# Optimization experiments

Measured on AMD Instinct MI355X. Metric: run time of the kernel, lower is better.

Reference implementation:

```python
import jax, jax.numpy as jnp
import numpy as np

HIDDEN = 2048
VOCAB = 32768
SEQ = 4608
N_CHUNKS = 9
CAP = 30.0
IGNORE = -100


def setup_inputs() -> dict:
    key = jax.random.key(0)
    k1, k2, k3 = jax.random.split(key, 3)
    weight = (jax.random.normal(k1, (VOCAB, HIDDEN), dtype=jnp.float32) * 0.02).astype(jnp.bfloat16)
    hidden = jax.random.normal(k2, (1, SEQ, HIDDEN), dtype=jnp.float32)
    input_ids = jax.random.randint(k3, (1, SEQ), 0, VOCAB)
    attention_mask = jnp.ones((1, SEQ), dtype=jnp.int32)
    return {"weight": weight, "hidden": hidden, "input_ids": input_ids,
            "attention_mask": attention_mask}


def _build_labels(input_ids, attention_mask):
    # labels[t] = input_ids[t+1], masked-out positions and the final position -> -100
    ids = input_ids[0]
    am = attention_mask[0]
    lab = jnp.where(am[1:] == 0, IGNORE, ids[1:])            # [S-1]
    lab = jnp.concatenate([lab, jnp.full((1,), IGNORE, lab.dtype)])  # [S]
    return lab


def reference(weight, hidden, input_ids, attention_mask):
    labels = _build_labels(input_ids, attention_mask)        # [S]
    x = hidden.reshape(-1, HIDDEN)                           # [S, H] fp32
    chunk = SEQ // N_CHUNKS
    xs = x.reshape(N_CHUNKS, chunk, HIDDEN)
    ls = labels.reshape(N_CHUNKS, chunk)

    wT = weight.T                                            # [H, V] bf16

    def chunk_loss(args):
        xc, lc = args                                        # [c,H], [c]
        # softcapped logits: CAP * tanh((x @ W^T) / CAP), mm in bf16
        t = jnp.tanh((xc.astype(jnp.bfloat16) @ wT) / CAP).astype(jnp.float32)  # [c,V]
        z = CAP * (t - jnp.max(t, axis=1, keepdims=True))    # stable shifted logits
        logp = z - jnp.log(jnp.sum(jnp.exp(z), axis=1, keepdims=True))
        valid = lc != IGNORE
        idx = jnp.where(valid, lc, 0)
        nll = -jnp.take_along_axis(logp, idx[:, None], axis=1)[:, 0]
        return jnp.sum(jnp.where(valid, nll, 0.0))

    losses = jax.lax.map(chunk_loss, (xs, ls))               # [N_CHUNKS]
    return jnp.sum(losses)
```

## Files before the change

### kernel.cpp

```cpp
#include <hip/hip_runtime.h>
#include <hip/hip_bf16.h>
#include <cstdint>

#define S_LEN   4608
#define HID     2048
#define VOCAB_N 32768
#define CAPV    30.0f
#define IGNORE_IDX (-100)
#define NT512   512
#define NKT     32

typedef short bf16x8 __attribute__((ext_vector_type(8)));
typedef float f32x4  __attribute__((ext_vector_type(4)));

__device__ __forceinline__ unsigned short f2bf_rtne(float f) {
    unsigned int u = __float_as_uint(f);
    unsigned int r = u + 0x7fffu + ((u >> 16) & 1u);
    return (unsigned short)(r >> 16);
}
__device__ __forceinline__ float bfr(float f) {
    unsigned int u = __float_as_uint(f);
    unsigned int r = u + 0x7fffu + ((u >> 16) & 1u);
    return __uint_as_float(r & 0xffff0000u);
}
__device__ __forceinline__ float bf_lo(unsigned int u) { return __uint_as_float(u << 16); }
__device__ __forceinline__ float bf_hi(unsigned int u) { return __uint_as_float(u & 0xffff0000u); }
__device__ __forceinline__ float bfdot2(unsigned int x, unsigned int w) {
    return bf_lo(x) * bf_lo(w) + bf_hi(x) * bf_hi(w);
}
__device__ __forceinline__ float softcap_ref(float logit) {
    float lb = bfr(logit);
    float x  = bfr(lb / CAPV);
    float e  = __expf(2.0f * x);
    float t  = bfr((e - 1.0f) / (e + 1.0f));
    return CAPV * t;
}

__global__ void cvt_kernel(const float* __restrict__ h, unsigned short* __restrict__ xb,
                           float* __restrict__ out) {
    if (blockIdx.x == 0 && threadIdx.x == 0) out[0] = 0.0f;
    int i = blockIdx.x * blockDim.x + threadIdx.x;
    float4 v = ((const float4*)h)[i];
    ushort4 o;
    o.x = f2bf_rtne(v.x); o.y = f2bf_rtne(v.y);
    o.z = f2bf_rtne(v.z); o.w = f2bf_rtne(v.w);
    ((ushort4*)xb)[i] = o;
}

__global__ __launch_bounds__(512, 2)
void gemm_lse_kernel(const unsigned short* __restrict__ X,
                     const unsigned short* __restrict__ W,
                     float* __restrict__ partL) {
    __shared__ __align__(16) unsigned short As[2][256 * 64];
    __shared__ __align__(16) unsigned short Bs[2][256 * 64];

    const int tid  = threadIdx.x;
    const int wid  = tid >> 6;
    const int lane = tid & 63;
    const int wr   = wid >> 2;
    const int wc   = wid & 3;
    const int q    = lane >> 4, l16 = lane & 15;
    const int tileM = blockIdx.x * 256;
    const int tileN = blockIdx.y * 256;

    const int srow = lane >> 3;
    const int csrc = (lane & 7) ^ srow;
    const unsigned short* Ag = X + (size_t)(tileM + wid * 8 + srow) * HID + csrc * 8;
    const unsigned short* Wg = W + (size_t)(tileN + wid * 8 + srow) * HID + csrc * 8;

    const int abase = (wr * 128 + l16) * 64;
    const int bbase = (wc * 64  + l16) * 64;
    const int koff0 = ((q    ) ^ (l16 & 7)) * 8;
    const int koff1 = ((q + 4) ^ (l16 & 7)) * 8;

    bf16x8 av[8][2], bv[4][2];
    f32x4  acc[8][4] = {};

#define STAGE_A(BUF, H, KT) do {                                                          \
    const unsigned short* _g = Ag + (size_t)(H) * 128 * HID + (size_t)(KT) * 64;          \
    __builtin_amdgcn_global_load_lds(                                                     \
        (const __attribute__((address_space(1))) void*)_g,                                \
        (__attribute__((address_space(3))) void*)&As[BUF][((H) * 128 + wid * 8) * 64],    \
        16, 0, 0);                                                                        \
    __builtin_amdgcn_global_load_lds(                                                     \
        (const __attribute__((address_space(1))) void*)(_g + (size_t)64 * HID),           \
        (__attribute__((address_space(3))) void*)&As[BUF][((H) * 128 + 64 + wid * 8) * 64],\
        16, 0, 0);                                                                        \
} while (0)

#define STAGE_B(BUF, H, KT) do {                                                          \
    const unsigned short* _g = Wg + (size_t)(H) * 128 * HID + (size_t)(KT) * 64;          \
    __builtin_amdgcn_global_load_lds(                                                     \
        (const __attribute__((address_space(1))) void*)_g,                                \
        (__attribute__((address_space(3))) void*)&Bs[BUF][((H) * 128 + wid * 8) * 64],    \
        16, 0, 0);                                                                        \
    __builtin_amdgcn_global_load_lds(                                                     \
        (const __attribute__((address_space(1))) void*)(_g + (size_t)64 * HID),           \
        (__attribute__((address_space(3))) void*)&Bs[BUF][((H) * 128 + 64 + wid * 8) * 64],\
        16, 0, 0);                                                                        \
} while (0)

#define RD_A(BUF, MH) do {                                                                \
    _Pragma("unroll") for (int fm = 0; fm < 4; ++fm) {                                    \
        av[(MH) * 4 + fm][0] = *(const bf16x8*)&As[BUF][abase + ((MH) * 64 + fm * 16) * 64 + koff0]; \
        av[(MH) * 4 + fm][1] = *(const bf16x8*)&As[BUF][abase + ((MH) * 64 + fm * 16) * 64 + koff1]; \
    } } while (0)

#define RD_B(BUF, NH) do {                                                                \
    _Pragma("unroll") for (int fn = 0; fn < 2; ++fn) {                                    \
        bv[(NH) * 2 + fn][0] = *(const bf16x8*)&Bs[BUF][bbase + ((NH) * 32 + fn * 16) * 64 + koff0]; \
        bv[(NH) * 2 + fn][1] = *(const bf16x8*)&Bs[BUF][bbase + ((NH) * 32 + fn * 16) * 64 + koff1]; \
    } } while (0)

#define MFMAQ(MH, NH) do {                                                                \
    _Pragma("unroll") for (int kk = 0; kk < 2; ++kk)                                      \
    _Pragma("unroll") for (int fm = 0; fm < 4; ++fm)                                      \
    _Pragma("unroll") for (int fn = 0; fn < 2; ++fn)                                      \
        acc[(MH) * 4 + fm][(NH) * 2 + fn] = __builtin_amdgcn_mfma_f32_16x16x32_bf16(      \
            av[(MH) * 4 + fm][kk], bv[(NH) * 2 + fn][kk],                                 \
            acc[(MH) * 4 + fm][(NH) * 2 + fn], 0, 0, 0);                                  \
} while (0)

#define BAR()   __builtin_amdgcn_s_barrier()
#define PRIO1() __builtin_amdgcn_s_setprio(1)
#define PRIO0() __builtin_amdgcn_s_setprio(0)
#define VMCNT8() asm volatile("s_waitcnt vmcnt(8)" ::: "memory")
#define VMCNT4() asm volatile("s_waitcnt vmcnt(4)" ::: "memory")
#define VMCNT0() asm volatile("s_waitcnt vmcnt(0)" ::: "memory")

#define KTILE(CUR, NXT, T) do {                                                           \
    RD_B(CUR, 1);                                                                         \
    BAR(); PRIO1(); MFMAQ(0, 0); PRIO0(); BAR();                                          \
    RD_A(CUR, 1); STAGE_B(CUR, 0, (T) + 2); STAGE_B(CUR, 1, (T) + 2);                     \
    BAR(); PRIO1(); MFMAQ(0, 1); PRIO0(); VMCNT4(); BAR();                                \
    RD_A(NXT, 0); STAGE_A(CUR, 0, (T) + 2); STAGE_A(CUR, 1, (T) + 2);                     \
    BAR(); PRIO1(); MFMAQ(1, 0); PRIO0(); BAR();                                          \
    RD_B(NXT, 0);                                                                         \
    BAR(); PRIO1(); MFMAQ(1, 1); PRIO0(); BAR();                                          \
} while (0)

    STAGE_B(0, 0, 0); STAGE_B(0, 1, 0);
    STAGE_A(0, 0, 0); STAGE_A(0, 1, 0);
    STAGE_B(1, 0, 1); STAGE_B(1, 1, 1);
    STAGE_A(1, 0, 1); STAGE_A(1, 1, 1);
    VMCNT8();
    BAR();
    RD_A(0, 0); RD_B(0, 0);

    #pragma unroll 1
    for (int t = 0; t < NKT - 2; t += 2) {
        KTILE(0, 1, t);
        KTILE(1, 0, t + 1);
    }

    RD_B(0, 1);
    BAR(); PRIO1(); MFMAQ(0, 0); PRIO0(); BAR();
    RD_A(0, 1);
    BAR(); PRIO1(); MFMAQ(0, 1); PRIO0(); VMCNT0(); BAR();
    RD_A(1, 0);
    BAR(); PRIO1(); MFMAQ(1, 0); PRIO0(); BAR();
    RD_B(1, 0);
    BAR(); PRIO1(); MFMAQ(1, 1); PRIO0(); BAR();

    RD_B(1, 1);
    PRIO1(); MFMAQ(0, 0); PRIO0();
    RD_A(1, 1);
    PRIO1(); MFMAQ(0, 1); PRIO0();
    PRIO1(); MFMAQ(1, 0); PRIO0();
    PRIO1(); MFMAQ(1, 1); PRIO0();

    const int rowbase = tileM + wr * 128;
    const int ntile   = blockIdx.y * 4 + wc;
    #pragma unroll
    for (int m = 0; m < 8; ++m) {
        #pragma unroll
        for (int r = 0; r < 4; ++r) {
            float s = 0.0f;
            #pragma unroll
            for (int n = 0; n < 4; ++n)
                s += __expf(softcap_ref(acc[m][n][r]));
            s += __shfl_xor(s, 1);
            s += __shfl_xor(s, 2);
            s += __shfl_xor(s, 4);
            s += __shfl_xor(s, 8);
            if (l16 == 0)
                partL[(size_t)(rowbase + m * 16 + q * 4 + r) * NT512 + ntile] = s;
        }
    }

#undef STAGE_A
#undef STAGE_B
#undef RD_A
#undef RD_B
#undef MFMAQ
#undef BAR
#undef PRIO1
#undef PRIO0
#undef VMCNT8
#undef VMCNT4
#undef VMCNT0
#undef KTILE
}

__global__ void row_reduce_kernel(const unsigned short* __restrict__ X,
                                  const unsigned short* __restrict__ W,
                                  const int* __restrict__ ids,
                                  const int* __restrict__ am,
                                  const float* __restrict__ partL,
                                  float* __restrict__ out) {
    __shared__ float blk[4];
    const int wave = threadIdx.x >> 6;
    const int lane = threadIdx.x & 63;
    const int r = blockIdx.x * 4 + wave;

    int lab = IGNORE_IDX;
    if (r < S_LEN - 1 && am[r + 1] != 0) lab = ids[r + 1];
    const bool valid = (lab >= 0 && lab < VOCAB_N);

    float dot = 0.0f;
    if (valid) {
        const unsigned short* xr = X + (size_t)r   * HID;
        const unsigned short* wr = W + (size_t)lab * HID;
        #pragma unroll
        for (int c = 0; c < 4; ++c) {
            const int off = c * 512 + lane * 8;
            uint4 xu = *(const uint4*)(xr + off);
            uint4 wu = *(const uint4*)(wr + off);
            dot += bfdot2(xu.x, wu.x) + bfdot2(xu.y, wu.y) +
                   bfdot2(xu.z, wu.z) + bfdot2(xu.w, wu.w);
        }
    }
    #pragma unroll
    for (int m = 1; m < 64; m <<= 1) dot += __shfl_xor(dot, m);

    float L = 0.0f;
    const float* pr = partL + (size_t)r * NT512;
    #pragma unroll
    for (int i = 0; i < 8; ++i) L += pr[i * 64 + lane];
    #pragma unroll
    for (int m = 1; m < 64; m <<= 1) L += __shfl_xor(L, m);

    if (lane == 0) {
        float loss = 0.0f;
        if (valid) loss = logf(L) - softcap_ref(dot);
        blk[wave] = loss;
    }
    __syncthreads();
    if (threadIdx.x == 0)
        atomicAdd(out, blk[0] + blk[1] + blk[2] + blk[3]);
}

extern "C" void kernel_launch(void* const* d_in, const int* in_sizes, int n_in,
                              void* d_out, int out_size, void* d_ws, size_t ws_size,
                              hipStream_t stream) {
    const unsigned short* W  = (const unsigned short*)d_in[0];
    const float*  hidden     = (const float*)d_in[1];
    const int*    ids        = (const int*)d_in[2];
    const int*    am         = (const int*)d_in[3];
    float* out = (float*)d_out;

    char* ws = (char*)d_ws;
    unsigned short* Xb = (unsigned short*)ws;
    float* partL       = (float*)(ws + (size_t)S_LEN * HID * 2);

    cvt_kernel<<<(S_LEN * HID / 4) / 256, 256, 0, stream>>>(hidden, Xb, out);

    dim3 g(S_LEN / 256, VOCAB_N / 256);
    gemm_lse_kernel<<<g, 512, 0, stream>>>(Xb, W, partL);

    row_reduce_kernel<<<S_LEN / 4, 256, 0, stream>>>(Xb, W, ids, am, partL, out);
}
```

Before: 1.090 ms.

## Replace direct global-to-LDS loads with register-staged loads and LDS writes

The GEMM mainloop stops using global_load_lds DMA into LDS. Each tile is now loaded from global memory into registers and written to LDS with ds_write, and the loads, stores, LDS reads, MFMAs and barriers are rescheduled into one hand-interleaved loop body. The intent is to hide global latency behind MFMA work and drop the vmcnt waits tied to the direct-to-LDS path. The cost is 32 extra VGPRs for the staging registers and extra LDS write instructions, which may reduce occupancy or stall on the lgkmcnt waits.

```diff
diff --git a/kernel.cpp b/kernel.cpp
--- a/kernel.cpp
+++ b/kernel.cpp
@@ -12,6 +12,7 @@
 
 typedef short bf16x8 __attribute__((ext_vector_type(8)));
 typedef float f32x4  __attribute__((ext_vector_type(4)));
+typedef int   i32x4  __attribute__((ext_vector_type(4)));
 
 __device__ __forceinline__ unsigned short f2bf_rtne(float f) {
     unsigned int u = __float_as_uint(f);
@@ -67,6 +68,7 @@
     const int csrc = (lane & 7) ^ srow;
     const unsigned short* Ag = X + (size_t)(tileM + wid * 8 + srow) * HID + csrc * 8;
     const unsigned short* Wg = W + (size_t)(tileN + wid * 8 + srow) * HID + csrc * 8;
+    const int dsw_off = (wid * 8 + srow) * 64 + (lane & 7) * 8;
 
     const int abase = (wr * 128 + l16) * 64;
     const int bbase = (wc * 64  + l16) * 64;
@@ -74,30 +76,39 @@
     const int koff1 = ((q + 4) ^ (l16 & 7)) * 8;
 
     bf16x8 av[8][2], bv[4][2];
+    i32x4  Areg[4], Breg[4];
     f32x4  acc[8][4] = {};
 
-#define STAGE_A(BUF, H, KT) do {                                                          \
-    const unsigned short* _g = Ag + (size_t)(H) * 128 * HID + (size_t)(KT) * 64;          \
-    __builtin_amdgcn_global_load_lds(                                                     \
-        (const __attribute__((address_space(1))) void*)_g,                                \
-        (__attribute__((address_space(3))) void*)&As[BUF][((H) * 128 + wid * 8) * 64],    \
-        16, 0, 0);                                                                        \
-    __builtin_amdgcn_global_load_lds(                                                     \
-        (const __attribute__((address_space(1))) void*)(_g + (size_t)64 * HID),           \
-        (__attribute__((address_space(3))) void*)&As[BUF][((H) * 128 + 64 + wid * 8) * 64],\
-        16, 0, 0);                                                                        \
-} while (0)
-
-#define STAGE_B(BUF, H, KT) do {                                                          \
-    const unsigned short* _g = Wg + (size_t)(H) * 128 * HID + (size_t)(KT) * 64;          \
-    __builtin_amdgcn_global_load_lds(                                                     \
-        (const __attribute__((address_space(1))) void*)_g,                                \
-        (__attribute__((address_space(3))) void*)&Bs[BUF][((H) * 128 + wid * 8) * 64],    \
-        16, 0, 0);                                                                        \
-    __builtin_amdgcn_global_load_lds(                                                     \
-        (const __attribute__((address_space(1))) void*)(_g + (size_t)64 * HID),           \
-        (__attribute__((address_space(3))) void*)&Bs[BUF][((H) * 128 + 64 + wid * 8) * 64],\
-        16, 0, 0);                                                                        \
+#define GL_A(KT) do {                                                                     \
+    const unsigned short* _g = Ag + (size_t)(KT) * 64;                                    \
+    Areg[0] = *(const i32x4*)(_g);                                                        \
+    Areg[1] = *(const i32x4*)(_g + (size_t)64  * HID);                                    \
+    Areg[2] = *(const i32x4*)(_g + (size_t)128 * HID);                                    \
+    Areg[3] = *(const i32x4*)(_g + (size_t)192 * HID);                                    \
+} while (0)
+
+#define GL_B(KT) do {                                                                     \
+    const unsigned short* _g = Wg + (size_t)(KT) * 64;                                    \
+    Breg[0] = *(const i32x4*)(_g);                                                        \
+    Breg[1] = *(const i32x4*)(_g + (size_t)64  * HID);                                    \
+    Breg[2] = *(const i32x4*)(_g + (size_t)128 * HID);                                    \
+    Breg[3] = *(const i32x4*)(_g + (size_t)192 * HID);                                    \
+} while (0)
+
+#define DSW_A(BUF) do {                                                                   \
+    unsigned short* _l = &As[BUF][dsw_off];                                               \
+    *(i32x4*)(_l)            = Areg[0];                                                   \
+    *(i32x4*)(_l +  64 * 64) = Areg[1];                                                   \
+    *(i32x4*)(_l + 128 * 64) = Areg[2];                                                   \
+    *(i32x4*)(_l + 192 * 64) = Areg[3];                                                   \
+} while (0)
+
+#define DSW_B(BUF) do {                                                                   \
+    unsigned short* _l = &Bs[BUF][dsw_off];                                               \
+    *(i32x4*)(_l)            = Breg[0];                                                   \
+    *(i32x4*)(_l +  64 * 64) = Breg[1];                                                   \
+    *(i32x4*)(_l + 128 * 64) = Breg[2];                                                   \
+    *(i32x4*)(_l + 192 * 64) = Breg[3];                                                   \
 } while (0)
 
 #define RD_A(BUF, MH) do {                                                                \
@@ -124,43 +135,52 @@
 #define BAR()   __builtin_amdgcn_s_barrier()
 #define PRIO1() __builtin_amdgcn_s_setprio(1)
 #define PRIO0() __builtin_amdgcn_s_setprio(0)
-#define VMCNT8() asm volatile("s_waitcnt vmcnt(8)" ::: "memory")
-#define VMCNT4() asm volatile("s_waitcnt vmcnt(4)" ::: "memory")
-#define VMCNT0() asm volatile("s_waitcnt vmcnt(0)" ::: "memory")
-
-#define KTILE(CUR, NXT, T) do {                                                           \
-    RD_B(CUR, 1);                                                                         \
-    BAR(); PRIO1(); MFMAQ(0, 0); PRIO0(); BAR();                                          \
-    RD_A(CUR, 1); STAGE_B(CUR, 0, (T) + 2); STAGE_B(CUR, 1, (T) + 2);                     \
-    BAR(); PRIO1(); MFMAQ(0, 1); PRIO0(); VMCNT4(); BAR();                                \
-    RD_A(NXT, 0); STAGE_A(CUR, 0, (T) + 2); STAGE_A(CUR, 1, (T) + 2);                     \
-    BAR(); PRIO1(); MFMAQ(1, 0); PRIO0(); BAR();                                          \
-    RD_B(NXT, 0);                                                                         \
-    BAR(); PRIO1(); MFMAQ(1, 1); PRIO0(); BAR();                                          \
-} while (0)
-
-    STAGE_B(0, 0, 0); STAGE_B(0, 1, 0);
-    STAGE_A(0, 0, 0); STAGE_A(0, 1, 0);
-    STAGE_B(1, 0, 1); STAGE_B(1, 1, 1);
-    STAGE_A(1, 0, 1); STAGE_A(1, 1, 1);
-    VMCNT8();
+#define LGKM0() do { asm volatile("s_waitcnt lgkmcnt(0)" ::: "memory");                   \
+                     __builtin_amdgcn_sched_barrier(0); } while (0)
+
+    GL_B(0); GL_A(0);
+    DSW_B(0); DSW_A(0);
+    LGKM0(); BAR();
+    RD_A(0, 0); RD_B(0, 0);
+    GL_B(1);
     BAR();
-    RD_A(0, 0); RD_B(0, 0);
 
     #pragma unroll 1
     for (int t = 0; t < NKT - 2; t += 2) {
-        KTILE(0, 1, t);
-        KTILE(1, 0, t + 1);
+        RD_B(0, 1);
+        GL_A(t + 1);
+        PRIO1(); MFMAQ(0, 0); PRIO0(); BAR();
+        RD_A(0, 1);
+        PRIO1(); MFMAQ(0, 1); PRIO0(); BAR();
+        DSW_B(1); DSW_A(1);
+        PRIO1(); MFMAQ(1, 0); PRIO0();
+        LGKM0(); BAR();
+        RD_A(1, 0); RD_B(1, 0);
+        GL_B(t + 2);
+        PRIO1(); MFMAQ(1, 1); PRIO0(); BAR();
+        RD_B(1, 1);
+        GL_A(t + 2);
+        PRIO1(); MFMAQ(0, 0); PRIO0(); BAR();
+        RD_A(1, 1);
+        PRIO1(); MFMAQ(0, 1); PRIO0(); BAR();
+        DSW_B(0); DSW_A(0);
+        PRIO1(); MFMAQ(1, 0); PRIO0();
+        LGKM0(); BAR();
+        RD_A(0, 0); RD_B(0, 0);
+        GL_B(t + 3);
+        PRIO1(); MFMAQ(1, 1); PRIO0(); BAR();
     }
 
     RD_B(0, 1);
-    BAR(); PRIO1(); MFMAQ(0, 0); PRIO0(); BAR();
+    GL_A(31);
+    PRIO1(); MFMAQ(0, 0); PRIO0(); BAR();
     RD_A(0, 1);
-    BAR(); PRIO1(); MFMAQ(0, 1); PRIO0(); VMCNT0(); BAR();
-    RD_A(1, 0);
-    BAR(); PRIO1(); MFMAQ(1, 0); PRIO0(); BAR();
-    RD_B(1, 0);
-    BAR(); PRIO1(); MFMAQ(1, 1); PRIO0(); BAR();
+    PRIO1(); MFMAQ(0, 1); PRIO0(); BAR();
+    DSW_B(1); DSW_A(1);
+    PRIO1(); MFMAQ(1, 0); PRIO0();
+    LGKM0(); BAR();
+    RD_A(1, 0); RD_B(1, 0);
+    PRIO1(); MFMAQ(1, 1); PRIO0(); BAR();
 
     RD_B(1, 1);
     PRIO1(); MFMAQ(0, 0); PRIO0();
@@ -188,18 +208,17 @@
         }
     }
 
-#undef STAGE_A
-#undef STAGE_B
+#undef GL_A
+#undef GL_B
+#undef DSW_A
+#undef DSW_B
 #undef RD_A
 #undef RD_B
 #undef MFMAQ
 #undef BAR
 #undef PRIO1
 #undef PRIO0
-#undef VMCNT8
-#undef VMCNT4
-#undef VMCNT0
-#undef KTILE
+#undef LGKM0
 }
 
 __global__ void row_reduce_kernel(const unsigned short* __restrict__ X,
```

New measurement: 2.469 ms. 127% more time.
